# Kernel optimization log

Measured on AMD Instinct MI355X. Metric: run time of the kernel, lower is better.

Reference implementation:

```python
import jax, jax.numpy as jnp
import numpy as np

V, E, H, TAGS, T = 100000, 300, 512, 25, 2048
NEG = -10000.0


def _lstm_dir(x, w_ih, w_hh, b_ih, b_hh, reverse):
    # x: [T, din]; PyTorch gate order i, f, g, o. Single sequence (batch=1 squeezed).
    def step(carry, xt):
        h, c = carry
        gates = xt @ w_ih.T + b_ih + h @ w_hh.T + b_hh  # [4H]
        i_, f_, g_, o_ = jnp.split(gates, 4)
        i_ = jax.nn.sigmoid(i_)
        f_ = jax.nn.sigmoid(f_)
        g_ = jnp.tanh(g_)
        o_ = jax.nn.sigmoid(o_)
        c = f_ * c + i_ * g_
        h = o_ * jnp.tanh(c)
        return (h, c), h
    h0 = jnp.zeros((H,), x.dtype)
    _, hs = jax.lax.scan(step, (h0, h0), x, reverse=reverse)
    return hs  # [T, H]


def _bilstm_layer(x, wf_ih, wf_hh, bf_ih, bf_hh, wb_ih, wb_hh, bb_ih, bb_hh):
    hf = _lstm_dir(x, wf_ih, wf_hh, bf_ih, bf_hh, reverse=False)
    hb = _lstm_dir(x, wb_ih, wb_hh, bb_ih, bb_hh, reverse=True)
    return jnp.concatenate([hf, hb], axis=-1)  # [T, 2H]


def _viterbi(feats, transitions):
    # feats: [T, TAGS]; transitions[next, prev]
    fv0 = jnp.full((TAGS,), NEG, feats.dtype).at[0].set(0.0)

    def vstep(fv, feat):
        scores = fv[None, :] + transitions        # [next, prev]
        bp = jnp.argmax(scores, axis=1)            # [TAGS]
        fv = jnp.max(scores, axis=1) + feat        # [TAGS]
        return fv, bp

    fv, bps = jax.lax.scan(vstep, fv0, feats)      # bps: [T, TAGS]
    best = jnp.argmax(fv)

    def back(tag, bp):
        return bp[tag], tag

    _, path = jax.lax.scan(back, best, bps, reverse=True)
    return path  # [T] int tags, times 0..T-1


def setup_inputs() -> dict:
    key = jax.random.key(0)
    ks = jax.random.split(key, 24)

    def g(k, shape, scale=0.05):
        return jax.random.normal(k, shape, dtype=jnp.float32) * scale

    inp = {}
    inp["sentence"] = jax.random.randint(ks[0], (1, T), 0, V)
    inp["embedding"] = g(ks[1], (V, E))
    i = 2
    for layer, din in ((0, E), (1, 2 * H)):
        for d in ("f", "b"):
            inp[f"w_ih_l{layer}_{d}"] = g(ks[i], (4 * H, din)); i += 1
            inp[f"w_hh_l{layer}_{d}"] = g(ks[i], (4 * H, H)); i += 1
            inp[f"b_ih_l{layer}_{d}"] = g(ks[i], (4 * H,)); i += 1
            inp[f"b_hh_l{layer}_{d}"] = g(ks[i], (4 * H,)); i += 1
    inp["w_tag"] = g(ks[18], (TAGS, 2 * H))
    inp["b_tag"] = g(ks[19], (TAGS,))
    inp["transitions"] = jax.random.normal(ks[20], (TAGS, TAGS), dtype=jnp.float32)
    return inp


def reference(sentence, embedding,
              w_ih_l0_f, w_hh_l0_f, b_ih_l0_f, b_hh_l0_f,
              w_ih_l0_b, w_hh_l0_b, b_ih_l0_b, b_hh_l0_b,
              w_ih_l1_f, w_hh_l1_f, b_ih_l1_f, b_hh_l1_f,
              w_ih_l1_b, w_hh_l1_b, b_ih_l1_b, b_hh_l1_b,
              w_tag, b_tag, transitions):
    x = embedding[sentence[0]]  # [T, E] (batch=1, squeezed as in original)
    h1 = _bilstm_layer(x, w_ih_l0_f, w_hh_l0_f, b_ih_l0_f, b_hh_l0_f,
                       w_ih_l0_b, w_hh_l0_b, b_ih_l0_b, b_hh_l0_b)
    h2 = _bilstm_layer(h1, w_ih_l1_f, w_hh_l1_f, b_ih_l1_f, b_hh_l1_f,
                       w_ih_l1_b, w_hh_l1_b, b_ih_l1_b, b_hh_l1_b)
    feats = h2 @ w_tag.T + b_tag  # [T, TAGS]
    return _viterbi(feats, transitions)
```

## Files before the change

kernel.cpp:

```cpp
#include <hip/hip_runtime.h>
#include <cmath>

#define TT   2048
#define EE   300
#define HH   512
#define G4H  2048
#define NTAG 25
#define NEGV (-10000.0f)
#define POISON 0xFFBADBADu

__device__ __forceinline__ float fsig(float x)  { return 1.f / (1.f + __expf(-x)); }
__device__ __forceinline__ float ftanh(float x) { return 1.f - 2.f / (__expf(2.f * x) + 1.f); }
__device__ __forceinline__ uint32_t f2u(float x) { return __float_as_uint(x); }
__device__ __forceinline__ float u2f(uint32_t x) { return __uint_as_float(x); }

__global__ void poison_kernel(uint32_t* __restrict__ p, int n) {
    int i = blockIdx.x * blockDim.x + threadIdx.x;
    for (; i < n; i += gridDim.x * blockDim.x) p[i] = POISON;
}

__global__ void embed_kernel(const int* __restrict__ sent,
                             const float* __restrict__ emb,
                             float* __restrict__ x) {
    int t = blockIdx.x;
    int row = sent[t];
    const float4* src = (const float4*)(emb + (size_t)row * EE);
    float4* dst = (float4*)(x + (size_t)t * EE);
    for (int i = threadIdx.x; i < EE / 4; i += blockDim.x) dst[i] = src[i];
}

#define BM 64
#define BN 64
#define BKK 16
__global__ __launch_bounds__(256)
void gemm_abt(const float* __restrict__ A, int lda,
              const float* __restrict__ B, int ldb,
              const float* __restrict__ bias1,
              const float* __restrict__ bias2,
              float* __restrict__ C, int ldc,
              int M, int N, int K) {
    __shared__ float As[BKK][BM + 4];
    __shared__ float Bs[BKK][BN + 4];
    const int tid = threadIdx.x;
    const int tx = tid & 15, ty = tid >> 4;
    const int bm = blockIdx.x * BM, bn = blockIdx.y * BN;
    float acc[4][4] = {};
    for (int k0 = 0; k0 < K; k0 += BKK) {
        #pragma unroll
        for (int i = 0; i < 4; ++i) {
            int m = (tid >> 4) + i * 16;
            int k = tid & 15;
            float a = 0.f, b = 0.f;
            if (k0 + k < K) {
                if (bm + m < M) a = A[(size_t)(bm + m) * lda + k0 + k];
                if (bn + m < N) b = B[(size_t)(bn + m) * ldb + k0 + k];
            }
            As[k][m] = a;
            Bs[k][m] = b;
        }
        __syncthreads();
        #pragma unroll
        for (int k = 0; k < BKK; ++k) {
            float4 a4 = *(const float4*)&As[k][ty * 4];
            float4 b4 = *(const float4*)&Bs[k][tx * 4];
            acc[0][0] += a4.x * b4.x; acc[0][1] += a4.x * b4.y;
            acc[0][2] += a4.x * b4.z; acc[0][3] += a4.x * b4.w;
            acc[1][0] += a4.y * b4.x; acc[1][1] += a4.y * b4.y;
            acc[1][2] += a4.y * b4.z; acc[1][3] += a4.y * b4.w;
            acc[2][0] += a4.z * b4.x; acc[2][1] += a4.z * b4.y;
            acc[2][2] += a4.z * b4.z; acc[2][3] += a4.z * b4.w;
            acc[3][0] += a4.w * b4.x; acc[3][1] += a4.w * b4.y;
            acc[3][2] += a4.w * b4.z; acc[3][3] += a4.w * b4.w;
        }
        __syncthreads();
    }
    #pragma unroll
    for (int i = 0; i < 4; ++i) {
        int m = bm + ty * 4 + i;
        if (m < M) {
            #pragma unroll
            for (int j = 0; j < 4; ++j) {
                int n = bn + tx * 4 + j;
                if (n < N) {
                    float v = acc[i][j];
                    if (bias1) v += bias1[n];
                    if (bias2) v += bias2[n];
                    C[(size_t)m * ldc + n] = v;
                }
            }
        }
    }
}

#define GM 128
#define GN 128
#define GK 16
__global__ __launch_bounds__(256)
void gemm128(const float* __restrict__ A, int lda,
             const float* __restrict__ B, int ldb,
             const float* __restrict__ bias1,
             const float* __restrict__ bias2,
             float* __restrict__ C, int ldc, int K) {
    __shared__ float As[GK][GM + 4];
    __shared__ float Bs[GK][GN + 4];
    const int tid = threadIdx.x;
    const int tx = tid & 15, ty = tid >> 4;
    const int bm = blockIdx.x * GM, bn = blockIdx.y * GN;
    const int lm = tid >> 1, lkq = (tid & 1) * 8;
    float acc[8][8] = {};
    for (int k0 = 0; k0 < K; k0 += GK) {
        float4 a0 = *(const float4*)&A[(size_t)(bm + lm) * lda + k0 + lkq];
        float4 a1 = *(const float4*)&A[(size_t)(bm + lm) * lda + k0 + lkq + 4];
        float4 b0 = *(const float4*)&B[(size_t)(bn + lm) * ldb + k0 + lkq];
        float4 b1 = *(const float4*)&B[(size_t)(bn + lm) * ldb + k0 + lkq + 4];
        As[lkq + 0][lm] = a0.x; As[lkq + 1][lm] = a0.y;
        As[lkq + 2][lm] = a0.z; As[lkq + 3][lm] = a0.w;
        As[lkq + 4][lm] = a1.x; As[lkq + 5][lm] = a1.y;
        As[lkq + 6][lm] = a1.z; As[lkq + 7][lm] = a1.w;
        Bs[lkq + 0][lm] = b0.x; Bs[lkq + 1][lm] = b0.y;
        Bs[lkq + 2][lm] = b0.z; Bs[lkq + 3][lm] = b0.w;
        Bs[lkq + 4][lm] = b1.x; Bs[lkq + 5][lm] = b1.y;
        Bs[lkq + 6][lm] = b1.z; Bs[lkq + 7][lm] = b1.w;
        __syncthreads();
        #pragma unroll
        for (int k = 0; k < GK; ++k) {
            float4 x0 = *(const float4*)&As[k][ty * 8];
            float4 x1 = *(const float4*)&As[k][ty * 8 + 4];
            float4 y0 = *(const float4*)&Bs[k][tx * 8];
            float4 y1 = *(const float4*)&Bs[k][tx * 8 + 4];
            float xa[8] = {x0.x, x0.y, x0.z, x0.w, x1.x, x1.y, x1.z, x1.w};
            float yb[8] = {y0.x, y0.y, y0.z, y0.w, y1.x, y1.y, y1.z, y1.w};
            #pragma unroll
            for (int i = 0; i < 8; ++i)
                #pragma unroll
                for (int j = 0; j < 8; ++j)
                    acc[i][j] += xa[i] * yb[j];
        }
        __syncthreads();
    }
    #pragma unroll
    for (int i = 0; i < 8; ++i) {
        int m = bm + ty * 8 + i;
        float* cr = C + (size_t)m * ldc + bn + tx * 8;
        #pragma unroll
        for (int j = 0; j < 8; ++j) {
            float v = acc[i][j];
            int n = bn + tx * 8 + j;
            if (bias1) v += bias1[n];
            if (bias2) v += bias2[n];
            cr[j] = v;
        }
    }
}

__global__ __launch_bounds__(512, 1)
void lstm_kernel(const float* __restrict__ gx,
                 const float* __restrict__ whh_f,
                 const float* __restrict__ whh_b,
                 float* __restrict__ gates,
                 float* __restrict__ hout)
{
    const int tid = threadIdx.x;
    const int dir = blockIdx.x >> 5;
    const int wg  = blockIdx.x & 31;
    const int r   = tid >> 3;
    const int cch = tid & 7;
    const int gb  = r >> 4;
    const int ur  = r & 15;
    const int grow = gb * HH + wg * 16 + ur;
    const float* W = dir ? whh_b : whh_f;

    float4 w[16];
    {
        const float4* wr = (const float4*)(W + (size_t)grow * HH);
        #pragma unroll
        for (int i = 0; i < 16; ++i) w[i] = wr[cch + 8 * i];
    }
    #pragma unroll
    for (int i = 0; i < 16; ++i) {
        asm volatile("v_mov_b32 %0, %0" : "+v"(w[i].x));
        asm volatile("v_mov_b32 %0, %0" : "+v"(w[i].y));
        asm volatile("v_mov_b32 %0, %0" : "+v"(w[i].z));
        asm volatile("v_mov_b32 %0, %0" : "+v"(w[i].w));
    }

    __shared__ float h_s[HH];

    float c = 0.f;
    uint32_t* gbuf = (uint32_t*)(gates + (size_t)dir * TT * G4H);
    const float* gxd = gx + (size_t)dir * TT * G4H;

    float gxc = 0.f, gxn = 0.f, gxf = 0.f;
    if (cch == 0) {
        int t0 = dir ? TT - 1 : 0;
        int t1 = dir ? TT - 2 : 1;
        gxc = gxd[(size_t)t0 * G4H + grow];
        gxn = gxd[(size_t)t1 * G4H + grow];
    }

    for (int s = 0; s <= TT; ++s) {
        if (s > 0) {
            const uint32_t* gp = gbuf + (size_t)(s - 1) * G4H + tid;
            uint32_t v0, v1, v2, v3;
            for (;;) {
                v0 = __hip_atomic_load(gp,        __ATOMIC_RELAXED, __HIP_MEMORY_SCOPE_AGENT);
                v1 = __hip_atomic_load(gp + 512,  __ATOMIC_RELAXED, __HIP_MEMORY_SCOPE_AGENT);
                v2 = __hip_atomic_load(gp + 1024, __ATOMIC_RELAXED, __HIP_MEMORY_SCOPE_AGENT);
                v3 = __hip_atomic_load(gp + 1536, __ATOMIC_RELAXED, __HIP_MEMORY_SCOPE_AGENT);
                if ((v0 != POISON) & (v1 != POISON) & (v2 != POISON) & (v3 != POISON)) break;
            }
            float gi = fsig(u2f(v0));
            float gf = fsig(u2f(v1));
            float gg = ftanh(u2f(v2));
            float go = fsig(u2f(v3));
            c = gf * c + gi * gg;
            float h = go * ftanh(c);
            h_s[tid] = h;
            if (wg == 0) {
                int tp = dir ? (TT - s) : (s - 1);
                hout[(size_t)tp * (2 * HH) + dir * HH + tid] = h;
            }
        } else {
            h_s[tid] = 0.f;
        }
        if (s == TT) break;

        if (cch == 0) {
            gxf = 0.f;
            if (s + 2 < TT) {
                int tf = dir ? (TT - 3 - s) : (s + 2);
                gxf = gxd[(size_t)tf * G4H + grow];
            }
        }
        __syncthreads();

        float a0 = 0.f, a1 = 0.f, a2 = 0.f, a3 = 0.f;
        const float4* h4 = (const float4*)h_s;
        #pragma unroll
        for (int i = 0; i < 16; i += 4) {
            float4 p0 = h4[cch + 8 * (i + 0)];
            float4 p1 = h4[cch + 8 * (i + 1)];
            float4 p2 = h4[cch + 8 * (i + 2)];
            float4 p3 = h4[cch + 8 * (i + 3)];
            a0 += w[i + 0].x * p0.x + w[i + 0].y * p0.y + w[i + 0].z * p0.z + w[i + 0].w * p0.w;
            a1 += w[i + 1].x * p1.x + w[i + 1].y * p1.y + w[i + 1].z * p1.z + w[i + 1].w * p1.w;
            a2 += w[i + 2].x * p2.x + w[i + 2].y * p2.y + w[i + 2].z * p2.z + w[i + 2].w * p2.w;
            a3 += w[i + 3].x * p3.x + w[i + 3].y * p3.y + w[i + 3].z * p3.z + w[i + 3].w * p3.w;
        }
        float acc = (a0 + a1) + (a2 + a3);
        acc += __shfl_xor(acc, 1);
        acc += __shfl_xor(acc, 2);
        acc += __shfl_xor(acc, 4);
        if (cch == 0)
            __hip_atomic_store(gbuf + (size_t)s * G4H + grow,
                               f2u(acc + gxc),
                               __ATOMIC_RELAXED, __HIP_MEMORY_SCOPE_AGENT);
        __syncthreads();
        gxc = gxn; gxn = gxf;
    }
}

__global__ void viterbi_kernel(const float* __restrict__ feats,
                               const float* __restrict__ trans,
                               int* __restrict__ out) {
    const int n = threadIdx.x;
    __shared__ float fv_s[NTAG];
    __shared__ uint8_t bp_s[TT][NTAG];
    float tr[NTAG];
    if (n < NTAG) {
        #pragma unroll
        for (int p = 0; p < NTAG; ++p) tr[p] = trans[n * NTAG + p];
    }
    float fv = (n == 0) ? 0.f : NEGV;
    float fcur = (n < NTAG) ? feats[n] : 0.f;
    for (int t = 0; t < TT; ++t) {
        float fnext = (n < NTAG && t + 1 < TT) ? feats[(t + 1) * NTAG + n] : 0.f;
        if (n < NTAG) fv_s[n] = fv;
        __syncthreads();
        if (n < NTAG) {
            float best = -INFINITY; int bb = 0;
            #pragma unroll
            for (int p = 0; p < NTAG; ++p) {
                float sc = fv_s[p] + tr[p];
                if (sc > best) { best = sc; bb = p; }
            }
            bp_s[t][n] = (uint8_t)bb;
            fv = best + fcur;
        }
        fcur = fnext;
        __syncthreads();
    }
    if (n < NTAG) fv_s[n] = fv;
    __syncthreads();
    if (n == 0) {
        float best = -INFINITY; int tag = 0;
        for (int p = 0; p < NTAG; ++p)
            if (fv_s[p] > best) { best = fv_s[p]; tag = p; }
        for (int t = TT - 1; t >= 0; --t) {
            out[t] = tag;
            tag = bp_s[t][tag];
        }
    }
}

extern "C" void kernel_launch(void* const* d_in, const int* in_sizes, int n_in,
                              void* d_out, int out_size, void* d_ws, size_t ws_size,
                              hipStream_t stream) {
    const int*   sent      = (const int*)d_in[0];
    const float* emb       = (const float*)d_in[1];
    const float* w_ih_l0_f = (const float*)d_in[2];
    const float* w_hh_l0_f = (const float*)d_in[3];
    const float* b_ih_l0_f = (const float*)d_in[4];
    const float* b_hh_l0_f = (const float*)d_in[5];
    const float* w_ih_l0_b = (const float*)d_in[6];
    const float* w_hh_l0_b = (const float*)d_in[7];
    const float* b_ih_l0_b = (const float*)d_in[8];
    const float* b_hh_l0_b = (const float*)d_in[9];
    const float* w_ih_l1_f = (const float*)d_in[10];
    const float* w_hh_l1_f = (const float*)d_in[11];
    const float* b_ih_l1_f = (const float*)d_in[12];
    const float* b_hh_l1_f = (const float*)d_in[13];
    const float* w_ih_l1_b = (const float*)d_in[14];
    const float* w_hh_l1_b = (const float*)d_in[15];
    const float* b_ih_l1_b = (const float*)d_in[16];
    const float* b_hh_l1_b = (const float*)d_in[17];
    const float* w_tag     = (const float*)d_in[18];
    const float* b_tag     = (const float*)d_in[19];
    const float* trans     = (const float*)d_in[20];

    char* ws = (char*)d_ws;
    float* x     = (float*)(ws);
    float* gx    = (float*)(ws + 2457600);
    float* gates = (float*)(ws + 36012032);
    float* h1    = (float*)(ws + 69566464);
    float* h2    = (float*)(ws + 77955072);
    float* feats = (float*)(ws + 86343680);

    const int NGATES = 2 * TT * G4H;

    poison_kernel<<<2048, 256, 0, stream>>>((uint32_t*)gates, NGATES);

    embed_kernel<<<TT, 128, 0, stream>>>(sent, emb, x);

    dim3 g0(TT / BM, G4H / BN);
    gemm_abt<<<g0, 256, 0, stream>>>(x, EE, w_ih_l0_f, EE, b_ih_l0_f, b_hh_l0_f,
                                     gx, G4H, TT, G4H, EE);
    gemm_abt<<<g0, 256, 0, stream>>>(x, EE, w_ih_l0_b, EE, b_ih_l0_b, b_hh_l0_b,
                                     gx + (size_t)TT * G4H, G4H, TT, G4H, EE);
    lstm_kernel<<<64, 512, 0, stream>>>(gx, w_hh_l0_f, w_hh_l0_b, gates, h1);

    dim3 g1(TT / GM, G4H / GN);
    gemm128<<<g1, 256, 0, stream>>>(h1, 2 * HH, w_ih_l1_f, 2 * HH, b_ih_l1_f, b_hh_l1_f,
                                    gx, G4H, 2 * HH);
    gemm128<<<g1, 256, 0, stream>>>(h1, 2 * HH, w_ih_l1_b, 2 * HH, b_ih_l1_b, b_hh_l1_b,
                                    gx + (size_t)TT * G4H, G4H, 2 * HH);
    poison_kernel<<<2048, 256, 0, stream>>>((uint32_t*)gates, NGATES);
    lstm_kernel<<<64, 512, 0, stream>>>(gx, w_hh_l1_f, w_hh_l1_b, gates, h2);

    dim3 gf(TT / BM, 1);
    gemm_abt<<<gf, 256, 0, stream>>>(h2, 2 * HH, w_tag, 2 * HH, b_tag, nullptr,
                                     feats, NTAG, TT, NTAG, 2 * HH);

    viterbi_kernel<<<1, 64, 0, stream>>>(feats, trans, (int*)d_out);
}
```

Before: 7.536 ms.

## Spread LSTM recurrence over 256 smaller workgroups with 16-lane row reductions

The persistent LSTM kernel moves from 64 blocks of 512 threads to 256 blocks of 256 threads. Each block now owns 4 rows per gate, with 16 lanes reducing each row, so every thread keeps 8 float4 weights instead of 16. Each thread also updates two hidden units per step and polls eight gate values. The aim is to use more CUs and cut per-thread matvec latency on the serial path. In exchange, each step needs more cross-block polling traffic through global memory, and the asm register pinning of the weights is dropped.

Result: slower. 9.343 ms (+24.0%).

```diff
diff --git a/kernel.cpp b/kernel.cpp
--- a/kernel.cpp
+++ b/kernel.cpp
@@ -153,7 +153,7 @@
     }
 }
 
-__global__ __launch_bounds__(512, 1)
+__global__ __launch_bounds__(256, 1)
 void lstm_kernel(const float* __restrict__ gx,
                  const float* __restrict__ whh_f,
                  const float* __restrict__ whh_b,
@@ -161,99 +161,98 @@
                  float* __restrict__ hout)
 {
     const int tid = threadIdx.x;
-    const int dir = blockIdx.x >> 5;
-    const int wg  = blockIdx.x & 31;
-    const int r   = tid >> 3;
-    const int cch = tid & 7;
-    const int gb  = r >> 4;
-    const int ur  = r & 15;
-    const int grow = gb * HH + wg * 16 + ur;
+    const int dir = blockIdx.x >> 7;
+    const int wg  = blockIdx.x & 127;
+    const int g   = tid >> 4;
+    const int l   = tid & 15;
+    const int gb  = g >> 2;
+    const int row = gb * HH + wg * 4 + (g & 3);
     const float* W = dir ? whh_b : whh_f;
 
-    float4 w[16];
+    float4 w[8];
     {
-        const float4* wr = (const float4*)(W + (size_t)grow * HH);
-        #pragma unroll
-        for (int i = 0; i < 16; ++i) w[i] = wr[cch + 8 * i];
-    }
-    #pragma unroll
-    for (int i = 0; i < 16; ++i) {
-        asm volatile("v_mov_b32 %0, %0" : "+v"(w[i].x));
-        asm volatile("v_mov_b32 %0, %0" : "+v"(w[i].y));
-        asm volatile("v_mov_b32 %0, %0" : "+v"(w[i].z));
-        asm volatile("v_mov_b32 %0, %0" : "+v"(w[i].w));
+        const float4* wr = (const float4*)(W + (size_t)row * HH);
+        #pragma unroll
+        for (int i = 0; i < 8; ++i) w[i] = wr[l + 16 * i];
     }
 
     __shared__ float h_s[HH];
 
-    float c = 0.f;
-    uint32_t* gbuf = (uint32_t*)(gates + (size_t)dir * TT * G4H);
+    float c0 = 0.f, c1 = 0.f;
+    float* gbuf = gates + (size_t)dir * TT * G4H;
     const float* gxd = gx + (size_t)dir * TT * G4H;
 
     float gxc = 0.f, gxn = 0.f, gxf = 0.f;
-    if (cch == 0) {
+    if (l == 0) {
         int t0 = dir ? TT - 1 : 0;
         int t1 = dir ? TT - 2 : 1;
-        gxc = gxd[(size_t)t0 * G4H + grow];
-        gxn = gxd[(size_t)t1 * G4H + grow];
+        gxc = gxd[(size_t)t0 * G4H + row];
+        gxn = gxd[(size_t)t1 * G4H + row];
     }
 
     for (int s = 0; s <= TT; ++s) {
         if (s > 0) {
-            const uint32_t* gp = gbuf + (size_t)(s - 1) * G4H + tid;
-            uint32_t v0, v1, v2, v3;
+            const float* gp = gbuf + (size_t)(s - 1) * G4H;
+            float f0, f1, f2, f3, f4, f5, f6, f7;
             for (;;) {
-                v0 = __hip_atomic_load(gp,        __ATOMIC_RELAXED, __HIP_MEMORY_SCOPE_AGENT);
-                v1 = __hip_atomic_load(gp + 512,  __ATOMIC_RELAXED, __HIP_MEMORY_SCOPE_AGENT);
-                v2 = __hip_atomic_load(gp + 1024, __ATOMIC_RELAXED, __HIP_MEMORY_SCOPE_AGENT);
-                v3 = __hip_atomic_load(gp + 1536, __ATOMIC_RELAXED, __HIP_MEMORY_SCOPE_AGENT);
-                if ((v0 != POISON) & (v1 != POISON) & (v2 != POISON) & (v3 != POISON)) break;
-            }
-            float gi = fsig(u2f(v0));
-            float gf = fsig(u2f(v1));
-            float gg = ftanh(u2f(v2));
-            float go = fsig(u2f(v3));
-            c = gf * c + gi * gg;
-            float h = go * ftanh(c);
-            h_s[tid] = h;
+                f0 = __hip_atomic_load(gp + tid,          __ATOMIC_RELAXED, __HIP_MEMORY_SCOPE_AGENT);
+                f1 = __hip_atomic_load(gp + tid + 512,    __ATOMIC_RELAXED, __HIP_MEMORY_SCOPE_AGENT);
+                f2 = __hip_atomic_load(gp + tid + 1024,   __ATOMIC_RELAXED, __HIP_MEMORY_SCOPE_AGENT);
+                f3 = __hip_atomic_load(gp + tid + 1536,   __ATOMIC_RELAXED, __HIP_MEMORY_SCOPE_AGENT);
+                f4 = __hip_atomic_load(gp + tid + 256,    __ATOMIC_RELAXED, __HIP_MEMORY_SCOPE_AGENT);
+                f5 = __hip_atomic_load(gp + tid + 768,    __ATOMIC_RELAXED, __HIP_MEMORY_SCOPE_AGENT);
+                f6 = __hip_atomic_load(gp + tid + 1280,   __ATOMIC_RELAXED, __HIP_MEMORY_SCOPE_AGENT);
+                f7 = __hip_atomic_load(gp + tid + 1792,   __ATOMIC_RELAXED, __HIP_MEMORY_SCOPE_AGENT);
+                if ((f2u(f0) != POISON) & (f2u(f1) != POISON) &
+                    (f2u(f2) != POISON) & (f2u(f3) != POISON) &
+                    (f2u(f4) != POISON) & (f2u(f5) != POISON) &
+                    (f2u(f6) != POISON) & (f2u(f7) != POISON)) break;
+            }
+            float gi = fsig(f0), gf = fsig(f1), gg = ftanh(f2), go = fsig(f3);
+            c0 = gf * c0 + gi * gg;
+            float h0 = go * ftanh(c0);
+            gi = fsig(f4); gf = fsig(f5); gg = ftanh(f6); go = fsig(f7);
+            c1 = gf * c1 + gi * gg;
+            float h1 = go * ftanh(c1);
+            h_s[tid]       = h0;
+            h_s[tid + 256] = h1;
             if (wg == 0) {
                 int tp = dir ? (TT - s) : (s - 1);
-                hout[(size_t)tp * (2 * HH) + dir * HH + tid] = h;
+                float* hp = hout + (size_t)tp * (2 * HH) + dir * HH;
+                hp[tid]       = h0;
+                hp[tid + 256] = h1;
             }
         } else {
             h_s[tid] = 0.f;
+            h_s[tid + 256] = 0.f;
         }
         if (s == TT) break;
 
-        if (cch == 0) {
+        if (l == 0) {
             gxf = 0.f;
             if (s + 2 < TT) {
                 int tf = dir ? (TT - 3 - s) : (s + 2);
-                gxf = gxd[(size_t)tf * G4H + grow];
-            }
-        }
-        __syncthreads();
-
-        float a0 = 0.f, a1 = 0.f, a2 = 0.f, a3 = 0.f;
+                gxf = gxd[(size_t)tf * G4H + row];
+            }
+        }
+        __syncthreads();
+
+        float a0 = 0.f, a1 = 0.f;
         const float4* h4 = (const float4*)h_s;
         #pragma unroll
-        for (int i = 0; i < 16; i += 4) {
-            float4 p0 = h4[cch + 8 * (i + 0)];
-            float4 p1 = h4[cch + 8 * (i + 1)];
-            float4 p2 = h4[cch + 8 * (i + 2)];
-            float4 p3 = h4[cch + 8 * (i + 3)];
+        for (int i = 0; i < 8; i += 2) {
+            float4 p0 = h4[l + 16 * (i + 0)];
+            float4 p1 = h4[l + 16 * (i + 1)];
             a0 += w[i + 0].x * p0.x + w[i + 0].y * p0.y + w[i + 0].z * p0.z + w[i + 0].w * p0.w;
             a1 += w[i + 1].x * p1.x + w[i + 1].y * p1.y + w[i + 1].z * p1.z + w[i + 1].w * p1.w;
-            a2 += w[i + 2].x * p2.x + w[i + 2].y * p2.y + w[i + 2].z * p2.z + w[i + 2].w * p2.w;
-            a3 += w[i + 3].x * p3.x + w[i + 3].y * p3.y + w[i + 3].z * p3.z + w[i + 3].w * p3.w;
-        }
-        float acc = (a0 + a1) + (a2 + a3);
+        }
+        float acc = a0 + a1;
         acc += __shfl_xor(acc, 1);
         acc += __shfl_xor(acc, 2);
         acc += __shfl_xor(acc, 4);
-        if (cch == 0)
-            __hip_atomic_store(gbuf + (size_t)s * G4H + grow,
-                               f2u(acc + gxc),
+        acc += __shfl_xor(acc, 8);
+        if (l == 0)
+            __hip_atomic_store(gbuf + (size_t)s * G4H + row, acc + gxc,
                                __ATOMIC_RELAXED, __HIP_MEMORY_SCOPE_AGENT);
         __syncthreads();
         gxc = gxn; gxn = gxf;
@@ -347,7 +346,7 @@
                                      gx, G4H, TT, G4H, EE);
     gemm_abt<<<g0, 256, 0, stream>>>(x, EE, w_ih_l0_b, EE, b_ih_l0_b, b_hh_l0_b,
                                      gx + (size_t)TT * G4H, G4H, TT, G4H, EE);
-    lstm_kernel<<<64, 512, 0, stream>>>(gx, w_hh_l0_f, w_hh_l0_b, gates, h1);
+    lstm_kernel<<<256, 256, 0, stream>>>(gx, w_hh_l0_f, w_hh_l0_b, gates, h1);
 
     dim3 g1(TT / GM, G4H / GN);
     gemm128<<<g1, 256, 0, stream>>>(h1, 2 * HH, w_ih_l1_f, 2 * HH, b_ih_l1_f, b_hh_l1_f,
@@ -355,7 +354,7 @@
     gemm128<<<g1, 256, 0, stream>>>(h1, 2 * HH, w_ih_l1_b, 2 * HH, b_ih_l1_b, b_hh_l1_b,
                                     gx + (size_t)TT * G4H, G4H, 2 * HH);
     poison_kernel<<<2048, 256, 0, stream>>>((uint32_t*)gates, NGATES);
-    lstm_kernel<<<64, 512, 0, stream>>>(gx, w_hh_l1_f, w_hh_l1_b, gates, h2);
+    lstm_kernel<<<256, 256, 0, stream>>>(gx, w_hh_l1_f, w_hh_l1_b, gates, h2);
 
     dim3 gf(TT / BM, 1);
     gemm_abt<<<gf, 256, 0, stream>>>(h2, 2 * HH, w_tag, 2 * HH, b_tag, nullptr,
```
